# Kernel tuning notes

Hardware: AMD Instinct MI355X
Metric: run time of the kernel (lower is better)

The kernel has to match this reference:

```python
import jax, jax.numpy as jnp
import numpy as np

FG_THRESH = 0.5

def _descriptors(fmap, scribbles):
    # fmap: [B, C, h, w]; scribbles: [B, I, H, W]
    B, C, h, w = fmap.shape
    I = scribbles.shape[1]
    # bilinear resize (align_corners=False == half-pixel, no antialias, like torch)
    sr = jax.image.resize(scribbles, (B, I, h, w), method='bilinear', antialias=False)
    mask = (sr > FG_THRESH).astype(fmap.dtype)                 # [B, I, h, w]
    cnt = mask.sum(axis=(-1, -2))                              # [B, I]
    ssum = jnp.einsum('bihw,bchw->bic', mask, fmap)            # masked sum over HW
    mean = ssum / jnp.maximum(cnt, 1.0)[..., None]             # [B, I, C]
    # fallback when a mask has no foreground pixels: feature at argmax of soft mask
    idx = jnp.argmax(sr.reshape(B, I, h * w), axis=-1)         # [B, I]
    fflat = fmap.reshape(B, C, h * w)
    fb = jnp.take_along_axis(fflat, idx[:, None, :], axis=2)   # [B, C, I]
    fb = fb.transpose(0, 2, 1)                                 # [B, I, C]
    return jnp.where((cnt > 0)[..., None], mean, fb)

def setup_inputs() -> dict:
    key = jax.random.key(0)
    k0, k1, k2, k3 = jax.random.split(key, 4)
    return {
        'feat0': jax.random.normal(k0, (8, 256, 128, 128), dtype=jnp.float32),
        'feat1': jax.random.normal(k1, (8, 256, 64, 64), dtype=jnp.float32),
        'feat2': jax.random.normal(k2, (8, 256, 32, 32), dtype=jnp.float32),
        'scribbles': jax.random.uniform(k3, (8, 16, 512, 512), dtype=jnp.float32),
    }

def reference(feat0, feat1, feat2, scribbles):
    # multi_scale=True, random_bg_queries=False: per-level masked mean pool,
    # then average descriptors across feature levels. Output: [B, I, C]
    d0 = _descriptors(feat0, scribbles)
    d1 = _descriptors(feat1, scribbles)
    d2 = _descriptors(feat2, scribbles)
    return (d0 + d1 + d2) / 3.0
```

## Files before the change

### kernel.cpp

```cpp
#include <hip/hip_runtime.h>
#include <stdint.h>

#define NB 8
#define NI 16
#define NC 256
#define SH 512
#define NCH 84

typedef __bf16 bf16x8 __attribute__((ext_vector_type(8)));
typedef float f32x4 __attribute__((ext_vector_type(4)));
typedef uint32_t u32x4 __attribute__((ext_vector_type(4)));

static const size_t OFF_SSP = 0;
static const size_t OFF_CNT = OFF_SSP + (size_t)NB * NCH * NI * NC * 4;
static const size_t OFF_KEY = OFF_CNT + (size_t)NB * NCH * NI * 4;
static const size_t WS_NEED = OFF_KEY + (size_t)NB * NCH * NI * 8;

__device__ __forceinline__ float4 ld4(const float* p) {
    return *reinterpret_cast<const float4*>(p);
}

template<int W, int S, int P>
__device__ __forceinline__ void do_chunk(const float* __restrict__ f,
                                         const float* __restrict__ scr,
                                         float* __restrict__ ssp,
                                         int* __restrict__ cntp,
                                         unsigned long long* __restrict__ keyp,
                                         int b, int chunk, int slot, int tid,
                                         uint16_t* __restrict__ lmask,
                                         int* __restrict__ lcnt,
                                         unsigned long long* __restrict__ lkey) {
    const int pix = chunk * 256 + tid;
    const int y = pix / W;
    const int x = pix - y * W;
    const int r0 = S * y + (S / 2 - 1);
    const int c0s = S * x + (S / 2 - 1);
    const int lane = tid & 63;
    const float* sb = scr + (size_t)b * NI * SH * SH + (size_t)r0 * SH;
    unsigned int mword = 0;
    for (int i = 0; i < NI; ++i) {
        const float* sp = sb + (size_t)i * SH * SH;
        float s4;
        if constexpr (S == 4) {
            float4 q0 = ld4(sp + (c0s - 1));
            float4 q1 = ld4(sp + SH + (c0s - 1));
            s4 = (q0.y + q0.z) + (q1.y + q1.z);
        } else {
            s4 = (sp[c0s] + sp[c0s + 1]) + (sp[SH + c0s] + sp[SH + c0s + 1]);
        }
        bool bit = s4 > 2.0f;
        mword |= bit ? (1u << i) : 0u;
        unsigned long long bal = __ballot(bit);
        if (lane == 0) atomicAdd(&lcnt[i], (int)__popcll(bal));
        if (bal == 0ull) {
            unsigned int srb = __float_as_uint(0.25f * s4);
            unsigned int mx = srb;
            #pragma unroll
            for (int off = 1; off < 64; off <<= 1) {
                unsigned int o = __shfl_xor(mx, off, 64);
                mx = (o > mx) ? o : mx;
            }
            unsigned long long win = __ballot(srb == mx);
            if (lane == 0) {
                int wl = __ffsll((unsigned long long)win) - 1;
                unsigned int wpix = (unsigned int)(chunk * 256 + (tid & ~63) + wl);
                unsigned long long key = (((unsigned long long)mx) << 32)
                                       | (unsigned long long)(0xFFFFFFFFu - wpix);
                atomicMax(&lkey[i], key);
            }
        }
    }
    lmask[tid] = (uint16_t)mword;
    __syncthreads();
    if (tid < NI) {
        cntp[slot * NI + tid] = lcnt[tid];
        keyp[slot * NI + tid] = lkey[tid];
    }

    const int wave = tid >> 6;
    const int kg = lane >> 4;
    const int cl = lane & 15;
    const int c0 = wave * 64;
    const int kb = chunk * 256;
    const uint16_t* lmp = lmask + kg * 8;
    const float* fp0 = f + ((size_t)b * NC + c0 + cl) * P + kb + kg * 8;
    f32x4 acc0 = {0.f, 0.f, 0.f, 0.f};
    f32x4 acc1 = {0.f, 0.f, 0.f, 0.f};
    f32x4 acc2 = {0.f, 0.f, 0.f, 0.f};
    f32x4 acc3 = {0.f, 0.f, 0.f, 0.f};
    #pragma unroll
    for (int ks = 0; ks < 8; ++ks) {
        const uint4 wA = *reinterpret_cast<const uint4*>(lmp + ks * 32);
        u32x4 au;
        au.x = ((wA.x >> cl) & 0x10001u) * 0x3F80u;
        au.y = ((wA.y >> cl) & 0x10001u) * 0x3F80u;
        au.z = ((wA.z >> cl) & 0x10001u) * 0x3F80u;
        au.w = ((wA.w >> cl) & 0x10001u) * 0x3F80u;
        const bf16x8 av = __builtin_bit_cast(bf16x8, au);
        const float* fk = fp0 + ks * 32;
        #pragma unroll
        for (int nt = 0; nt < 4; ++nt) {
            const float* fr = fk + (size_t)(nt * 16) * P;
            float4 v0 = ld4(fr);
            float4 v1 = ld4(fr + 4);
            bf16x8 bv;
            bv[0] = (__bf16)v0.x; bv[1] = (__bf16)v0.y;
            bv[2] = (__bf16)v0.z; bv[3] = (__bf16)v0.w;
            bv[4] = (__bf16)v1.x; bv[5] = (__bf16)v1.y;
            bv[6] = (__bf16)v1.z; bv[7] = (__bf16)v1.w;
            if (nt == 0) acc0 = __builtin_amdgcn_mfma_f32_16x16x32_bf16(av, bv, acc0, 0, 0, 0);
            if (nt == 1) acc1 = __builtin_amdgcn_mfma_f32_16x16x32_bf16(av, bv, acc1, 0, 0, 0);
            if (nt == 2) acc2 = __builtin_amdgcn_mfma_f32_16x16x32_bf16(av, bv, acc2, 0, 0, 0);
            if (nt == 3) acc3 = __builtin_amdgcn_mfma_f32_16x16x32_bf16(av, bv, acc3, 0, 0, 0);
        }
    }
    float* sb2 = ssp + (size_t)slot * (NI * NC);
    #pragma unroll
    for (int nt = 0; nt < 4; ++nt) {
        const f32x4 ac = (nt == 0) ? acc0 : (nt == 1) ? acc1 : (nt == 2) ? acc2 : acc3;
        const int c = c0 + nt * 16 + cl;
        #pragma unroll
        for (int r = 0; r < 4; ++r)
            sb2[(kg * 4 + r) * NC + c] = ac[r];
    }
}

__global__ __launch_bounds__(256) void fused_kernel(const float* __restrict__ f0,
                                                    const float* __restrict__ f1,
                                                    const float* __restrict__ f2,
                                                    const float* __restrict__ scr,
                                                    float* __restrict__ ssp,
                                                    int* __restrict__ cntp,
                                                    unsigned long long* __restrict__ keyp) {
    __shared__ __align__(16) uint16_t lmask[256];
    __shared__ int lcnt[NI];
    __shared__ unsigned long long lkey[NI];
    const int tid = threadIdx.x;
    const int b = blockIdx.y;
    const int bx = blockIdx.x;
    if (tid < NI) { lcnt[tid] = 0; lkey[tid] = 0ull; }
    __syncthreads();
    const int slot = b * NCH + bx;
    if (bx < 64) {
        do_chunk<128, 4, 16384>(f0, scr, ssp, cntp, keyp, b, bx, slot, tid, lmask, lcnt, lkey);
    } else if (bx < 80) {
        do_chunk<64, 8, 4096>(f1, scr, ssp, cntp, keyp, b, bx - 64, slot, tid, lmask, lcnt, lkey);
    } else {
        do_chunk<32, 16, 1024>(f2, scr, ssp, cntp, keyp, b, bx - 80, slot, tid, lmask, lcnt, lkey);
    }
}

__global__ __launch_bounds__(256) void final_kernel(const float* __restrict__ f0,
                                                    const float* __restrict__ f1,
                                                    const float* __restrict__ f2,
                                                    const int* __restrict__ cntp,
                                                    const unsigned long long* __restrict__ keyp,
                                                    const float* __restrict__ ssp,
                                                    float* __restrict__ out) {
    __shared__ int scnt[3];
    __shared__ unsigned long long skey[3];
    const int bi = blockIdx.x;
    const int b = bi >> 4;
    const int i = bi & 15;
    const int tid = threadIdx.x;
    const int CH[3] = {64, 16, 4};
    const int O[3] = {0, 64, 80};
    if (tid < 64) {
        #pragma unroll
        for (int l = 0; l < 3; ++l) {
            int v = 0;
            unsigned long long k = 0ull;
            if (tid < CH[l]) {
                const int slot = b * NCH + O[l] + tid;
                v = cntp[slot * NI + i];
                k = keyp[slot * NI + i];
            }
            #pragma unroll
            for (int off = 32; off > 0; off >>= 1) {
                v += __shfl_down(v, off, 64);
                unsigned long long ko = __shfl_down(k, off, 64);
                k = (ko > k) ? ko : k;
            }
            if (tid == 0) { scnt[l] = v; skey[l] = k; }
        }
    }
    __syncthreads();
    const float* fl[3] = {f0, f1, f2};
    const int Ps[3] = {16384, 4096, 1024};
    const int c = tid;
    float r = 0.f;
    #pragma unroll
    for (int l = 0; l < 3; ++l) {
        const int cn = scnt[l];
        float v;
        if (cn > 0) {
            float s = 0.f;
            for (int j = 0; j < CH[l]; ++j)
                s += ssp[((size_t)(b * NCH + O[l] + j) * NI + i) * NC + c];
            v = s / (float)cn;
        } else {
            unsigned int p = 0xFFFFFFFFu - (unsigned int)(skey[l] & 0xFFFFFFFFull);
            v = fl[l][((size_t)b * NC + c) * Ps[l] + p];
        }
        r += v;
    }
    out[(size_t)bi * NC + c] = r * (1.f / 3.f);
}

extern "C" void kernel_launch(void* const* d_in, const int* in_sizes, int n_in,
                              void* d_out, int out_size, void* d_ws, size_t ws_size,
                              hipStream_t stream) {
    const float* f0  = (const float*)d_in[0];
    const float* f1  = (const float*)d_in[1];
    const float* f2  = (const float*)d_in[2];
    const float* scr = (const float*)d_in[3];
    float* out = (float*)d_out;
    char* ws = (char*)d_ws;
    if (ws_size < WS_NEED) return;

    float* ssp = (float*)(ws + OFF_SSP);
    int* cntp = (int*)(ws + OFF_CNT);
    unsigned long long* keyp = (unsigned long long*)(ws + OFF_KEY);

    fused_kernel<<<dim3(NCH, NB), 256, 0, stream>>>(f0, f1, f2, scr, ssp, cntp, keyp);
    final_kernel<<<NB * NI, NC, 0, stream>>>(f0, f1, f2, cntp, keyp, ssp, out);
}
```

Before: 65.13 us.

## Halve pixel chunk size and split instance loop across thread halves; parallelize final reduce

The fused kernel now processes 128 pixels per block instead of 256, doubling the grid to 168 blocks per batch. The two halves of each block each compute 8 of the 16 instance masks, and the 8-bit masks are merged in shared memory before the bf16 MFMA masked sum. The final kernel is split over 4 channel quarters, with 4 waves each reducing a strided subset of the (now doubled) partial sums. Both changes aim to raise parallelism and occupancy on the many-CU GPU, at the cost of twice as many partial sums to write and reduce, plus an extra barrier.

Result: slower. 75.42 us (+15.8%).

```diff
diff --git a/kernel.cpp b/kernel.cpp
--- a/kernel.cpp
+++ b/kernel.cpp
@@ -5,7 +5,7 @@
 #define NI 16
 #define NC 256
 #define SH 512
-#define NCH 84
+#define NCH 168
 
 typedef __bf16 bf16x8 __attribute__((ext_vector_type(8)));
 typedef float f32x4 __attribute__((ext_vector_type(4)));
@@ -27,19 +27,23 @@
                                          int* __restrict__ cntp,
                                          unsigned long long* __restrict__ keyp,
                                          int b, int chunk, int slot, int tid,
-                                         uint16_t* __restrict__ lmask,
+                                         uint8_t* __restrict__ lmask8,
+                                         uint16_t* __restrict__ lmask16,
                                          int* __restrict__ lcnt,
                                          unsigned long long* __restrict__ lkey) {
-    const int pix = chunk * 256 + tid;
+    const int gi = tid >> 7;
+    const int p = tid & 127;
+    const int pix = chunk * 128 + p;
     const int y = pix / W;
     const int x = pix - y * W;
     const int r0 = S * y + (S / 2 - 1);
     const int c0s = S * x + (S / 2 - 1);
     const int lane = tid & 63;
-    const float* sb = scr + (size_t)b * NI * SH * SH + (size_t)r0 * SH;
+    const float* sb = scr + ((size_t)b * NI + gi * 8) * (SH * SH) + (size_t)r0 * SH;
     unsigned int mword = 0;
-    for (int i = 0; i < NI; ++i) {
-        const float* sp = sb + (size_t)i * SH * SH;
+    #pragma unroll
+    for (int i = 0; i < 8; ++i) {
+        const float* sp = sb + (size_t)i * (SH * SH);
         float s4;
         if constexpr (S == 4) {
             float4 q0 = ld4(sp + (c0s - 1));
@@ -51,7 +55,7 @@
         bool bit = s4 > 2.0f;
         mword |= bit ? (1u << i) : 0u;
         unsigned long long bal = __ballot(bit);
-        if (lane == 0) atomicAdd(&lcnt[i], (int)__popcll(bal));
+        if (lane == 0) atomicAdd(&lcnt[gi * 8 + i], (int)__popcll(bal));
         if (bal == 0ull) {
             unsigned int srb = __float_as_uint(0.25f * s4);
             unsigned int mx = srb;
@@ -63,33 +67,36 @@
             unsigned long long win = __ballot(srb == mx);
             if (lane == 0) {
                 int wl = __ffsll((unsigned long long)win) - 1;
-                unsigned int wpix = (unsigned int)(chunk * 256 + (tid & ~63) + wl);
+                unsigned int wpix = (unsigned int)(chunk * 128 + (p & ~63) + wl);
                 unsigned long long key = (((unsigned long long)mx) << 32)
                                        | (unsigned long long)(0xFFFFFFFFu - wpix);
-                atomicMax(&lkey[i], key);
+                atomicMax(&lkey[gi * 8 + i], key);
             }
         }
     }
-    lmask[tid] = (uint16_t)mword;
-    __syncthreads();
+    lmask8[gi * 128 + p] = (uint8_t)mword;
+    __syncthreads();
+    if (tid < 128)
+        lmask16[tid] = (uint16_t)(lmask8[tid] | ((unsigned)lmask8[128 + tid] << 8));
     if (tid < NI) {
         cntp[slot * NI + tid] = lcnt[tid];
         keyp[slot * NI + tid] = lkey[tid];
     }
+    __syncthreads();
 
     const int wave = tid >> 6;
     const int kg = lane >> 4;
     const int cl = lane & 15;
     const int c0 = wave * 64;
-    const int kb = chunk * 256;
-    const uint16_t* lmp = lmask + kg * 8;
+    const int kb = chunk * 128;
+    const uint16_t* lmp = lmask16 + kg * 8;
     const float* fp0 = f + ((size_t)b * NC + c0 + cl) * P + kb + kg * 8;
     f32x4 acc0 = {0.f, 0.f, 0.f, 0.f};
     f32x4 acc1 = {0.f, 0.f, 0.f, 0.f};
     f32x4 acc2 = {0.f, 0.f, 0.f, 0.f};
     f32x4 acc3 = {0.f, 0.f, 0.f, 0.f};
     #pragma unroll
-    for (int ks = 0; ks < 8; ++ks) {
+    for (int ks = 0; ks < 4; ++ks) {
         const uint4 wA = *reinterpret_cast<const uint4*>(lmp + ks * 32);
         u32x4 au;
         au.x = ((wA.x >> cl) & 0x10001u) * 0x3F80u;
@@ -132,7 +139,8 @@
                                                     float* __restrict__ ssp,
                                                     int* __restrict__ cntp,
                                                     unsigned long long* __restrict__ keyp) {
-    __shared__ __align__(16) uint16_t lmask[256];
+    __shared__ uint8_t lmask8[256];
+    __shared__ __align__(16) uint16_t lmask16[128];
     __shared__ int lcnt[NI];
     __shared__ unsigned long long lkey[NI];
     const int tid = threadIdx.x;
@@ -141,12 +149,15 @@
     if (tid < NI) { lcnt[tid] = 0; lkey[tid] = 0ull; }
     __syncthreads();
     const int slot = b * NCH + bx;
-    if (bx < 64) {
-        do_chunk<128, 4, 16384>(f0, scr, ssp, cntp, keyp, b, bx, slot, tid, lmask, lcnt, lkey);
-    } else if (bx < 80) {
-        do_chunk<64, 8, 4096>(f1, scr, ssp, cntp, keyp, b, bx - 64, slot, tid, lmask, lcnt, lkey);
+    if (bx < 128) {
+        do_chunk<128, 4, 16384>(f0, scr, ssp, cntp, keyp, b, bx, slot, tid,
+                                lmask8, lmask16, lcnt, lkey);
+    } else if (bx < 160) {
+        do_chunk<64, 8, 4096>(f1, scr, ssp, cntp, keyp, b, bx - 128, slot, tid,
+                              lmask8, lmask16, lcnt, lkey);
     } else {
-        do_chunk<32, 16, 1024>(f2, scr, ssp, cntp, keyp, b, bx - 80, slot, tid, lmask, lcnt, lkey);
+        do_chunk<32, 16, 1024>(f2, scr, ssp, cntp, keyp, b, bx - 160, slot, tid,
+                               lmask8, lmask16, lcnt, lkey);
     }
 }
 
@@ -159,52 +170,46 @@
                                                     float* __restrict__ out) {
     __shared__ int scnt[3];
     __shared__ unsigned long long skey[3];
+    __shared__ float red[4][64];
     const int bi = blockIdx.x;
+    const int cq = blockIdx.y;
     const int b = bi >> 4;
     const int i = bi & 15;
     const int tid = threadIdx.x;
-    const int CH[3] = {64, 16, 4};
-    const int O[3] = {0, 64, 80};
-    if (tid < 64) {
-        #pragma unroll
-        for (int l = 0; l < 3; ++l) {
-            int v = 0;
-            unsigned long long k = 0ull;
-            if (tid < CH[l]) {
-                const int slot = b * NCH + O[l] + tid;
-                v = cntp[slot * NI + i];
-                k = keyp[slot * NI + i];
-            }
-            #pragma unroll
-            for (int off = 32; off > 0; off >>= 1) {
-                v += __shfl_down(v, off, 64);
-                unsigned long long ko = __shfl_down(k, off, 64);
-                k = (ko > k) ? ko : k;
-            }
-            if (tid == 0) { scnt[l] = v; skey[l] = k; }
-        }
+    const int cl = tid & 63;
+    const int jg = tid >> 6;
+    const int CH[3] = {128, 32, 8};
+    const int O[3] = {0, 128, 160};
+    if (tid < 3) { scnt[tid] = 0; skey[tid] = 0ull; }
+    __syncthreads();
+    if (tid < NCH) {
+        int l = (tid < 128) ? 0 : (tid < 160) ? 1 : 2;
+        const int slot = b * NCH + tid;
+        atomicAdd(&scnt[l], cntp[slot * NI + i]);
+        atomicMax(&skey[l], keyp[slot * NI + i]);
     }
     __syncthreads();
     const float* fl[3] = {f0, f1, f2};
     const int Ps[3] = {16384, 4096, 1024};
-    const int c = tid;
     float r = 0.f;
     #pragma unroll
     for (int l = 0; l < 3; ++l) {
         const int cn = scnt[l];
-        float v;
         if (cn > 0) {
             float s = 0.f;
-            for (int j = 0; j < CH[l]; ++j)
-                s += ssp[((size_t)(b * NCH + O[l] + j) * NI + i) * NC + c];
-            v = s / (float)cn;
-        } else {
+            for (int j = jg; j < CH[l]; j += 4)
+                s += ssp[((size_t)(b * NCH + O[l] + j) * NI + i) * NC + cq * 64 + cl];
+            red[jg][cl] = s;
+            __syncthreads();
+            if (jg == 0)
+                r += ((red[0][cl] + red[1][cl]) + (red[2][cl] + red[3][cl])) / (float)cn;
+            __syncthreads();
+        } else if (jg == 0) {
             unsigned int p = 0xFFFFFFFFu - (unsigned int)(skey[l] & 0xFFFFFFFFull);
-            v = fl[l][((size_t)b * NC + c) * Ps[l] + p];
-        }
-        r += v;
-    }
-    out[(size_t)bi * NC + c] = r * (1.f / 3.f);
+            r += fl[l][((size_t)b * NC + cq * 64 + cl) * Ps[l] + p];
+        }
+    }
+    if (jg == 0) out[(size_t)bi * NC + cq * 64 + cl] = r * (1.f / 3.f);
 }
 
 extern "C" void kernel_launch(void* const* d_in, const int* in_sizes, int n_in,
@@ -223,5 +228,5 @@
     unsigned long long* keyp = (unsigned long long*)(ws + OFF_KEY);
 
     fused_kernel<<<dim3(NCH, NB), 256, 0, stream>>>(f0, f1, f2, scr, ssp, cntp, keyp);
-    final_kernel<<<NB * NI, NC, 0, stream>>>(f0, f1, f2, cntp, keyp, ssp, out);
-}
+    final_kernel<<<dim3(NB * NI, 4), 256, 0, stream>>>(f0, f1, f2, cntp, keyp, ssp, out);
+}
```
